# Optimization experiments

Hardware: AMD Instinct MI355X
Metric: run time of the kernel (lower is better)

The kernel has to match this reference:

```python
import jax, jax.numpy as jnp
import numpy as np


def gcn_conv(x, W, b, src, dst, dinv_sqrt, n_nodes):
    # PyG GCNConv: h = X W; out_i = sum_j norm_ij * h_j + b, norm = d_i^-1/2 d_j^-1/2
    h = x @ W  # [N, out]
    norm = dinv_sqrt[src] * dinv_sqrt[dst]  # [E]
    msg = h[src] * norm[:, None]  # [E, out]
    out = jax.ops.segment_sum(msg, dst, num_segments=n_nodes)
    return out + b


def setup_inputs() -> dict:
    key = jax.random.key(0)
    ks = jax.random.split(key, 12)
    N, E, G = 50000, 400000, 512
    x = jax.random.normal(ks[0], (N, 3), dtype=jnp.float32)
    edge_index = jax.random.randint(ks[1], (2, E), 0, N, dtype=jnp.int64)
    batch = jnp.sort(jax.random.randint(ks[2], (N,), 0, G, dtype=jnp.int64))
    def lin(k, fin, fout):
        kw, kb = jax.random.split(k)
        s = 1.0 / np.sqrt(fin)
        return (jax.random.uniform(kw, (fin, fout), jnp.float32, -s, s),
                jax.random.uniform(kb, (fout,), jnp.float32, -s, s))
    W1, b1 = lin(ks[3], 3, 100)
    W2, b2 = lin(ks[4], 100, 200)
    W3, b3 = lin(ks[5], 200, 100)
    W4, b4 = lin(ks[6], 100, 1)
    return {"x": x, "edge_index": edge_index, "batch": batch, "num_graphs": G,
            "W1": W1, "b1": b1, "W2": W2, "b2": b2,
            "W3": W3, "b3": b3, "W4": W4, "b4": b4}


def reference(x, edge_index, batch, num_graphs, W1, b1, W2, b2, W3, b3, W4, b4):
    N = x.shape[0]
    loop = jnp.arange(N, dtype=edge_index.dtype)
    src = jnp.concatenate([edge_index[0], loop])  # self-loops added (GCNConv default)
    dst = jnp.concatenate([edge_index[1], loop])
    deg = jax.ops.segment_sum(jnp.ones_like(src, dtype=x.dtype), dst, num_segments=N)
    dinv_sqrt = deg ** -0.5  # deg >= 1 due to self-loops

    h = jax.nn.silu(gcn_conv(x, W1, b1, src, dst, dinv_sqrt, N))
    h = jax.nn.silu(gcn_conv(h, W2, b2, src, dst, dinv_sqrt, N))

    # global_mean_pool over `batch` segments
    sums = jax.ops.segment_sum(h, batch, num_segments=num_graphs)  # [G, 200]
    cnts = jax.ops.segment_sum(jnp.ones((N,), h.dtype), batch, num_segments=num_graphs)
    pooled = sums / jnp.maximum(cnts, 1.0)[:, None]

    h = jax.nn.silu(pooled @ W3 + b3)
    out = h @ W4 + b4  # [G, 1]
    return out.squeeze(-1)
```

## Files before the change

kernel.cpp:

```cpp
#include <hip/hip_runtime.h>
#include <math.h>

#define WF 64

__device__ __forceinline__ float silu_f(float v){ return v / (1.0f + expf(-v)); }

typedef __attribute__((ext_vector_type(8))) short bf16x8;
typedef __attribute__((ext_vector_type(4))) float f32x4;

__device__ __forceinline__ void bf16split(float v, unsigned short& h, unsigned short& l){
  unsigned int b = __float_as_uint(v);
  unsigned int hh = (b + 0x8000u) >> 16;
  float hf = __uint_as_float(hh << 16);
  float lo = v - hf;
  unsigned int bl = __float_as_uint(lo);
  h = (unsigned short)hh;
  l = (unsigned short)((bl + 0x8000u) >> 16);
}

__global__ __launch_bounds__(256) void k_count(const int* __restrict__ dst, int* __restrict__ cnt, int E){
  int e = blockIdx.x*blockDim.x + threadIdx.x;
  if (e < E) atomicAdd(&cnt[dst[e]], 1);
}

__global__ __launch_bounds__(256) void k_scan1(const int* __restrict__ cnt, int* __restrict__ rowstart, int* __restrict__ bsum, int N){
  __shared__ int s[256];
  int tid = threadIdx.x;
  int base = blockIdx.x*2048 + tid*8;
  int loc[8]; int tsum = 0;
#pragma unroll
  for (int j=0;j<8;++j){ int idx=base+j; int v = (idx<N)?cnt[idx]:0; loc[j]=tsum; tsum+=v; }
  s[tid]=tsum; __syncthreads();
  for (int off=1; off<256; off<<=1){
    int v = (tid>=off)? s[tid-off] : 0;
    __syncthreads();
    s[tid] += v;
    __syncthreads();
  }
  int texc = s[tid] - tsum;
  if (tid==255) bsum[blockIdx.x] = s[255];
#pragma unroll
  for (int j=0;j<8;++j){ int idx=base+j; if (idx<N) rowstart[idx] = texc + loc[j]; }
}

__global__ __launch_bounds__(256) void k_scan3(const int* __restrict__ bsum, const int* __restrict__ cnt,
                        const float* __restrict__ x,
                        int* __restrict__ rowstart, int* __restrict__ cursor,
                        float* __restrict__ dinv, float4* __restrict__ dxp,
                        int N, int E, int nb){
  __shared__ int boffs;
  int tid = threadIdx.x;
  int b = (blockIdx.x*blockDim.x) >> 11;
  if (tid < WF){
    int v = (tid < nb && tid < b) ? bsum[tid] : 0;
#pragma unroll
    for (int off=32; off; off>>=1) v += __shfl_down(v, off);
    if (tid==0) boffs = v;
  }
  __syncthreads();
  int idx = blockIdx.x*blockDim.x + tid;
  if (idx < N){
    int v = rowstart[idx] + boffs;
    rowstart[idx]=v; cursor[idx]=v;
    float di = rsqrtf((float)(cnt[idx]+1));
    dinv[idx] = di;
    float4 o;
    o.x = di;
    o.y = di*x[3*idx+0];
    o.z = di*x[3*idx+1];
    o.w = di*x[3*idx+2];
    dxp[idx] = o;
  }
  if (idx==0) rowstart[N]=E;
}

__global__ __launch_bounds__(256) void k_fill(const int* __restrict__ src, const int* __restrict__ dst,
                       int* __restrict__ cursor, int* __restrict__ colsrc, int E){
  int e = blockIdx.x*blockDim.x + threadIdx.x;
  if (e < E){
    int d = dst[e];
    int pos = atomicAdd(&cursor[d], 1);
    colsrc[pos] = src[e];
  }
}

__global__ __launch_bounds__(256) void k_wconv(const float* __restrict__ W2,
                       unsigned short* __restrict__ w2th, unsigned short* __restrict__ w2tl){
  int idx = blockIdx.x*blockDim.x + threadIdx.x;
  if (idx < 224*128){
    int f = idx >> 7, k = idx & 127;
    float v = (f < 200 && k < 100) ? W2[(size_t)k*200 + f] : 0.f;
    unsigned short h, l;
    bf16split(v, h, l);
    w2th[idx] = h;
    w2tl[idx] = l;
  }
}

__global__ __launch_bounds__(256) void k_l1(const float4* __restrict__ dxp,
                     const int* __restrict__ rowstart, const int* __restrict__ colsrc,
                     const float* __restrict__ W1, const float* __restrict__ b1,
                     float* __restrict__ h1s, int N){
  __shared__ float w[300];
  __shared__ float bb[100];
  int tid = threadIdx.x;
  for (int t=tid; t<300; t+=blockDim.x) w[t]=W1[t];
  for (int t=tid; t<100; t+=blockDim.x) bb[t]=b1[t];
  __syncthreads();
  int i = blockIdx.x*blockDim.x + tid;
  if (i >= N) return;
  float4 self = dxp[i];
  float di = self.x;
  float sx = self.y, sy = self.z, sz = self.w;
  int jb = rowstart[i], je = rowstart[i+1];
  int j = jb;
  for (; j+3 < je; j += 4){
    float4 r0 = dxp[colsrc[j]];
    float4 r1 = dxp[colsrc[j+1]];
    float4 r2 = dxp[colsrc[j+2]];
    float4 r3 = dxp[colsrc[j+3]];
    sx += (r0.y + r1.y) + (r2.y + r3.y);
    sy += (r0.z + r1.z) + (r2.z + r3.z);
    sz += (r0.w + r1.w) + (r2.w + r3.w);
  }
  for (; j < je; ++j){
    float4 r = dxp[colsrc[j]];
    sx += r.y; sy += r.z; sz += r.w;
  }
  sx*=di; sy*=di; sz*=di;
  float* orow = h1s + (size_t)i*100;
#pragma unroll
  for (int f0=0; f0<100; f0+=4){
    float4 o;
    o.x = silu_f(sx*w[f0+0] + sy*w[100+f0+0] + sz*w[200+f0+0] + bb[f0+0]);
    o.y = silu_f(sx*w[f0+1] + sy*w[100+f0+1] + sz*w[200+f0+1] + bb[f0+1]);
    o.z = silu_f(sx*w[f0+2] + sy*w[100+f0+2] + sz*w[200+f0+2] + bb[f0+2]);
    o.w = silu_f(sx*w[f0+3] + sy*w[100+f0+3] + sz*w[200+f0+3] + bb[f0+3]);
    *(float4*)&orow[f0] = o;
  }
}

__global__ __launch_bounds__(256) void k_agg2(const float* __restrict__ h1s, const int* __restrict__ rowstart,
                       const int* __restrict__ colsrc, const float* __restrict__ dinv,
                       unsigned short* __restrict__ a2h, unsigned short* __restrict__ a2l, int N){
  int node = blockIdx.x*8 + (threadIdx.x >> 5);
  int lane = threadIdx.x & 31;
  if (node >= N) return;
  if (lane >= 25){
    int ko = 100 + (lane-25)*4;
    ushort4 z = make_ushort4(0,0,0,0);
    *(ushort4*)(a2h + (size_t)node*128 + ko) = z;
    *(ushort4*)(a2l + (size_t)node*128 + ko) = z;
    return;
  }
  float di = dinv[node];
  float4 v = *(const float4*)(h1s + (size_t)node*100 + lane*4);
  float4 acc;
  acc.x = di*v.x; acc.y = di*v.y; acc.z = di*v.z; acc.w = di*v.w;
  int jb = rowstart[node], je = rowstart[node+1];
  int j = jb;
  for (; j+1 < je; j += 2){
    int u0 = colsrc[j];   float w0 = dinv[u0];
    int u1 = colsrc[j+1]; float w1 = dinv[u1];
    float4 r0 = *(const float4*)(h1s + (size_t)u0*100 + lane*4);
    float4 r1 = *(const float4*)(h1s + (size_t)u1*100 + lane*4);
    acc.x += w0*r0.x + w1*r1.x;
    acc.y += w0*r0.y + w1*r1.y;
    acc.z += w0*r0.z + w1*r1.z;
    acc.w += w0*r0.w + w1*r1.w;
  }
  if (j < je){
    int u = colsrc[j]; float wv = dinv[u];
    float4 r = *(const float4*)(h1s + (size_t)u*100 + lane*4);
    acc.x += wv*r.x; acc.y += wv*r.y; acc.z += wv*r.z; acc.w += wv*r.w;
  }
  float o[4] = { di*acc.x, di*acc.y, di*acc.z, di*acc.w };
  ushort4 h4, l4;
  bf16split(o[0], h4.x, l4.x);
  bf16split(o[1], h4.y, l4.y);
  bf16split(o[2], h4.z, l4.z);
  bf16split(o[3], h4.w, l4.w);
  *(ushort4*)(a2h + (size_t)node*128 + lane*4) = h4;
  *(ushort4*)(a2l + (size_t)node*128 + lane*4) = l4;
}

__global__ __launch_bounds__(256) void k_mm2(const unsigned short* __restrict__ a2h,
                      const unsigned short* __restrict__ a2l,
                      const unsigned short* __restrict__ w2th,
                      const unsigned short* __restrict__ w2tl,
                      const float* __restrict__ b2, const int* __restrict__ batch,
                      float* __restrict__ pooled, int N){
  __shared__ float plL[256];
  int tid = threadIdx.x;
  int l = tid & 63, w = tid >> 6;
  int n0 = blockIdx.x * 64;
  int fb = blockIdx.y;
  int row = l & 15;
  int kg  = l >> 4;

  const unsigned short* ah_p = a2h + (size_t)(n0 + w*16 + row)*128;
  const unsigned short* al_p = a2l + (size_t)(n0 + w*16 + row)*128;
  int gf0 = fb*32 + row, gf1 = gf0 + 16;
  const unsigned short* wh0_p = w2th + (size_t)gf0*128;
  const unsigned short* wl0_p = w2tl + (size_t)gf0*128;
  const unsigned short* wh1_p = w2th + (size_t)gf1*128;
  const unsigned short* wl1_p = w2tl + (size_t)gf1*128;

  f32x4 acc0 = {0.f,0.f,0.f,0.f};
  f32x4 acc1 = {0.f,0.f,0.f,0.f};
#pragma unroll
  for (int ks = 0; ks < 4; ++ks){
    int ko = ks*32 + kg*8;
    bf16x8 ah  = *(const bf16x8*)(ah_p  + ko);
    bf16x8 al  = *(const bf16x8*)(al_p  + ko);
    bf16x8 wh0 = *(const bf16x8*)(wh0_p + ko);
    bf16x8 wl0 = *(const bf16x8*)(wl0_p + ko);
    bf16x8 wh1 = *(const bf16x8*)(wh1_p + ko);
    bf16x8 wl1 = *(const bf16x8*)(wl1_p + ko);
    acc0 = __builtin_amdgcn_mfma_f32_16x16x32_bf16(ah, wh0, acc0, 0, 0, 0);
    acc0 = __builtin_amdgcn_mfma_f32_16x16x32_bf16(ah, wl0, acc0, 0, 0, 0);
    acc0 = __builtin_amdgcn_mfma_f32_16x16x32_bf16(al, wh0, acc0, 0, 0, 0);
    acc1 = __builtin_amdgcn_mfma_f32_16x16x32_bf16(ah, wh1, acc1, 0, 0, 0);
    acc1 = __builtin_amdgcn_mfma_f32_16x16x32_bf16(ah, wl1, acc1, 0, 0, 0);
    acc1 = __builtin_amdgcn_mfma_f32_16x16x32_bf16(al, wh1, acc1, 0, 0, 0);
  }

  plL[tid] = 0.f;
  __syncthreads();

  int g0 = batch[n0];
#pragma unroll
  for (int ft = 0; ft < 2; ++ft){
    f32x4 a = ft ? acc1 : acc0;
    int fl = ft*16 + row;
    int gf = fb*32 + fl;
    if (gf < 200){
      float bias = b2[gf];
      float s = 0.f;
      int gprev = -1;
#pragma unroll
      for (int r = 0; r < 4; ++r){
        int node = n0 + w*16 + kg*4 + r;
        if (node < N){
          int g = batch[node];
          if (g != gprev){
            if (gprev >= 0){
              int dg = gprev - g0;
              if (dg < 8) atomicAdd(&plL[dg*32 + fl], s);
              else        atomicAdd(&pooled[(size_t)gprev*200 + gf], s);
            }
            gprev = g; s = 0.f;
          }
          s += silu_f(a[r] + bias);
        }
      }
      if (gprev >= 0){
        int dg = gprev - g0;
        if (dg < 8) atomicAdd(&plL[dg*32 + fl], s);
        else        atomicAdd(&pooled[(size_t)gprev*200 + gf], s);
      }
    }
  }
  __syncthreads();
  {
    float v = plL[tid];
    if (v != 0.f){
      int r = tid >> 5, f = tid & 31;
      int gf = fb*32 + f;
      if (gf < 200) atomicAdd(&pooled[(size_t)(g0+r)*200 + gf], v);
    }
  }
}

__global__ __launch_bounds__(256) void k_head(const float* __restrict__ pooled, const int* __restrict__ batch,
                       const float* __restrict__ W3, const float* __restrict__ b3,
                       const float* __restrict__ W4, const float* __restrict__ b4,
                       float* __restrict__ out, int N){
  __shared__ float pl[200];
  __shared__ float h3[100];
  int g = blockIdx.x; int tid = threadIdx.x;
  int lo=0, hi=N;
  while (lo<hi){ int m=(lo+hi)>>1; if (batch[m] < g) lo=m+1; else hi=m; }
  int s = lo;
  hi=N;
  while (lo<hi){ int m=(lo+hi)>>1; if (batch[m] < g+1) lo=m+1; else hi=m; }
  int e = lo;
  float inv = (e>s) ? 1.0f/(float)(e-s) : 0.0f;
  if (tid < 200) pl[tid] = pooled[(size_t)g*200 + tid] * inv;
  __syncthreads();
  if (tid < 100){
    float acc = b3[tid];
    for (int k=0;k<200;++k) acc += pl[k]*W3[k*100+tid];
    h3[tid] = silu_f(acc);
  }
  __syncthreads();
  if (tid < WF){
    float p = 0.f;
    if (tid < 100)      p  = h3[tid]     * W4[tid];
    if (tid + 64 < 100) p += h3[tid+64]  * W4[tid+64];
#pragma unroll
    for (int off=32; off; off>>=1) p += __shfl_down(p, off);
    if (tid==0) out[g] = p + b4[0];
  }
}

extern "C" void kernel_launch(void* const* d_in, const int* in_sizes, int n_in,
                              void* d_out, int out_size, void* d_ws, size_t ws_size,
                              hipStream_t stream){
  const float* x  = (const float*)d_in[0];
  const int*   ei = (const int*)  d_in[1];
  const int* batch= (const int*)  d_in[2];
  const float* W1 = (const float*)d_in[4];
  const float* b1 = (const float*)d_in[5];
  const float* W2 = (const float*)d_in[6];
  const float* b2 = (const float*)d_in[7];
  const float* W3 = (const float*)d_in[8];
  const float* b3 = (const float*)d_in[9];
  const float* W4 = (const float*)d_in[10];
  const float* b4 = (const float*)d_in[11];
  float* out = (float*)d_out;

  int N = in_sizes[0]/3;
  int E = in_sizes[1]/2;
  int G = out_size;
  const int* src = ei;
  const int* dst = ei + E;
  int NP = ((N + 63)/64)*64;

  char* base = (char*)d_ws; size_t off = 0;
  auto alloc = [&](size_t bytes)->void*{
    void* p = base + off;
    off = (off + bytes + 255) & ~(size_t)255;
    return p;
  };
  int*   cnt      = (int*)  alloc((size_t)N*4);
  float* pooled   = (float*)alloc((size_t)G*200*4);
  size_t zbytes   = off;
  int*   rowstart = (int*)  alloc((size_t)(N+1)*4);
  int*   cursor   = (int*)  alloc((size_t)N*4);
  int*   bsum     = (int*)  alloc(4096);
  int*   colsrc   = (int*)  alloc((size_t)E*4);
  float* dinv     = (float*)alloc((size_t)N*4);
  float4* dxp     = (float4*)alloc((size_t)N*16);
  float* h1s      = (float*)alloc((size_t)N*100*4);
  unsigned short* a2h = (unsigned short*)alloc((size_t)NP*128*2);
  unsigned short* a2l = (unsigned short*)alloc((size_t)NP*128*2);
  unsigned short* w2th = (unsigned short*)alloc((size_t)224*128*2);
  unsigned short* w2tl = (unsigned short*)alloc((size_t)224*128*2);
  (void)ws_size; (void)n_in;

  hipMemsetAsync(base, 0, zbytes, stream);
  int gE = (E+255)/256;
  k_count<<<gE,256,0,stream>>>(dst, cnt, E);
  int nb = (N+2047)/2048;
  k_scan1<<<nb,256,0,stream>>>(cnt, rowstart, bsum, N);
  k_scan3<<<(N+255)/256,256,0,stream>>>(bsum, cnt, x, rowstart, cursor, dinv, dxp, N, E, nb);
  k_wconv<<<(224*128+255)/256,256,0,stream>>>(W2, w2th, w2tl);
  k_fill<<<gE,256,0,stream>>>(src, dst, cursor, colsrc, E);
  k_l1<<<(N+255)/256,256,0,stream>>>(dxp, rowstart, colsrc, W1, b1, h1s, N);
  k_agg2<<<(N+7)/8,256,0,stream>>>(h1s, rowstart, colsrc, dinv, a2h, a2l, N);
  dim3 gmm((N+63)/64, 7);
  k_mm2<<<gmm,256,0,stream>>>(a2h, a2l, w2th, w2tl, b2, batch, pooled, N);
  k_head<<<G,256,0,stream>>>(pooled, batch, W3, b3, W4, b4, out, N);
}
```

Measured before the change: 182.4 us.

## Loop over all feature blocks in k_mm2 to reuse A fragments in registers

k_mm2 used to launch a 2D grid where each block handled 64 nodes by one 32-feature slice, so every feature slice reloaded the a2h/a2l activation rows from global memory. Each 128-thread block now handles 32 nodes, loads their A fragments into registers once, and loops over all 7 feature blocks. Weight fragments are reloaded per iteration from the small, cache-resident W2 arrays. The cost is a serial loop with extra barriers per feature block and fewer total blocks, which reduces parallelism and latency hiding.

```diff
diff --git a/kernel.cpp b/kernel.cpp
--- a/kernel.cpp
+++ b/kernel.cpp
@@ -184,7 +184,7 @@
   *(ushort4*)(a2l + (size_t)node*128 + lane*4) = l4;
 }
 
-__global__ __launch_bounds__(256) void k_mm2(const unsigned short* __restrict__ a2h,
+__global__ __launch_bounds__(128) void k_mm2(const unsigned short* __restrict__ a2h,
                       const unsigned short* __restrict__ a2l,
                       const unsigned short* __restrict__ w2th,
                       const unsigned short* __restrict__ w2tl,
@@ -193,81 +193,91 @@
   __shared__ float plL[256];
   int tid = threadIdx.x;
   int l = tid & 63, w = tid >> 6;
-  int n0 = blockIdx.x * 64;
-  int fb = blockIdx.y;
+  int n0 = blockIdx.x * 32;
   int row = l & 15;
   int kg  = l >> 4;
 
   const unsigned short* ah_p = a2h + (size_t)(n0 + w*16 + row)*128;
   const unsigned short* al_p = a2l + (size_t)(n0 + w*16 + row)*128;
-  int gf0 = fb*32 + row, gf1 = gf0 + 16;
-  const unsigned short* wh0_p = w2th + (size_t)gf0*128;
-  const unsigned short* wl0_p = w2tl + (size_t)gf0*128;
-  const unsigned short* wh1_p = w2th + (size_t)gf1*128;
-  const unsigned short* wl1_p = w2tl + (size_t)gf1*128;
-
-  f32x4 acc0 = {0.f,0.f,0.f,0.f};
-  f32x4 acc1 = {0.f,0.f,0.f,0.f};
+
+  bf16x8 ahf[4], alf[4];
 #pragma unroll
   for (int ks = 0; ks < 4; ++ks){
     int ko = ks*32 + kg*8;
-    bf16x8 ah  = *(const bf16x8*)(ah_p  + ko);
-    bf16x8 al  = *(const bf16x8*)(al_p  + ko);
-    bf16x8 wh0 = *(const bf16x8*)(wh0_p + ko);
-    bf16x8 wl0 = *(const bf16x8*)(wl0_p + ko);
-    bf16x8 wh1 = *(const bf16x8*)(wh1_p + ko);
-    bf16x8 wl1 = *(const bf16x8*)(wl1_p + ko);
-    acc0 = __builtin_amdgcn_mfma_f32_16x16x32_bf16(ah, wh0, acc0, 0, 0, 0);
-    acc0 = __builtin_amdgcn_mfma_f32_16x16x32_bf16(ah, wl0, acc0, 0, 0, 0);
-    acc0 = __builtin_amdgcn_mfma_f32_16x16x32_bf16(al, wh0, acc0, 0, 0, 0);
-    acc1 = __builtin_amdgcn_mfma_f32_16x16x32_bf16(ah, wh1, acc1, 0, 0, 0);
-    acc1 = __builtin_amdgcn_mfma_f32_16x16x32_bf16(ah, wl1, acc1, 0, 0, 0);
-    acc1 = __builtin_amdgcn_mfma_f32_16x16x32_bf16(al, wh1, acc1, 0, 0, 0);
-  }
-
-  plL[tid] = 0.f;
-  __syncthreads();
+    ahf[ks] = *(const bf16x8*)(ah_p + ko);
+    alf[ks] = *(const bf16x8*)(al_p + ko);
+  }
 
   int g0 = batch[n0];
-#pragma unroll
-  for (int ft = 0; ft < 2; ++ft){
-    f32x4 a = ft ? acc1 : acc0;
-    int fl = ft*16 + row;
-    int gf = fb*32 + fl;
-    if (gf < 200){
-      float bias = b2[gf];
-      float s = 0.f;
-      int gprev = -1;
-#pragma unroll
-      for (int r = 0; r < 4; ++r){
-        int node = n0 + w*16 + kg*4 + r;
-        if (node < N){
-          int g = batch[node];
-          if (g != gprev){
-            if (gprev >= 0){
-              int dg = gprev - g0;
-              if (dg < 8) atomicAdd(&plL[dg*32 + fl], s);
-              else        atomicAdd(&pooled[(size_t)gprev*200 + gf], s);
+
+  for (int fb = 0; fb < 7; ++fb){
+    int gf0 = fb*32 + row, gf1 = gf0 + 16;
+    const unsigned short* wh0_p = w2th + (size_t)gf0*128;
+    const unsigned short* wl0_p = w2tl + (size_t)gf0*128;
+    const unsigned short* wh1_p = w2th + (size_t)gf1*128;
+    const unsigned short* wl1_p = w2tl + (size_t)gf1*128;
+
+    f32x4 acc0 = {0.f,0.f,0.f,0.f};
+    f32x4 acc1 = {0.f,0.f,0.f,0.f};
+#pragma unroll
+    for (int ks = 0; ks < 4; ++ks){
+      int ko = ks*32 + kg*8;
+      bf16x8 wh0 = *(const bf16x8*)(wh0_p + ko);
+      bf16x8 wl0 = *(const bf16x8*)(wl0_p + ko);
+      bf16x8 wh1 = *(const bf16x8*)(wh1_p + ko);
+      bf16x8 wl1 = *(const bf16x8*)(wl1_p + ko);
+      acc0 = __builtin_amdgcn_mfma_f32_16x16x32_bf16(ahf[ks], wh0, acc0, 0, 0, 0);
+      acc0 = __builtin_amdgcn_mfma_f32_16x16x32_bf16(ahf[ks], wl0, acc0, 0, 0, 0);
+      acc0 = __builtin_amdgcn_mfma_f32_16x16x32_bf16(alf[ks], wh0, acc0, 0, 0, 0);
+      acc1 = __builtin_amdgcn_mfma_f32_16x16x32_bf16(ahf[ks], wh1, acc1, 0, 0, 0);
+      acc1 = __builtin_amdgcn_mfma_f32_16x16x32_bf16(ahf[ks], wl1, acc1, 0, 0, 0);
+      acc1 = __builtin_amdgcn_mfma_f32_16x16x32_bf16(alf[ks], wh1, acc1, 0, 0, 0);
+    }
+
+    __syncthreads();
+    for (int idx = tid; idx < 256; idx += 128) plL[idx] = 0.f;
+    __syncthreads();
+
+#pragma unroll
+    for (int ft = 0; ft < 2; ++ft){
+      f32x4 a = ft ? acc1 : acc0;
+      int fl = ft*16 + row;
+      int gf = fb*32 + fl;
+      if (gf < 200){
+        float bias = b2[gf];
+        float s = 0.f;
+        int gprev = -1;
+#pragma unroll
+        for (int r = 0; r < 4; ++r){
+          int node = n0 + w*16 + kg*4 + r;
+          if (node < N){
+            int g = batch[node];
+            if (g != gprev){
+              if (gprev >= 0){
+                int dg = gprev - g0;
+                if (dg < 8) atomicAdd(&plL[dg*32 + fl], s);
+                else        atomicAdd(&pooled[(size_t)gprev*200 + gf], s);
+              }
+              gprev = g; s = 0.f;
             }
-            gprev = g; s = 0.f;
+            s += silu_f(a[r] + bias);
           }
-          s += silu_f(a[r] + bias);
+        }
+        if (gprev >= 0){
+          int dg = gprev - g0;
+          if (dg < 8) atomicAdd(&plL[dg*32 + fl], s);
+          else        atomicAdd(&pooled[(size_t)gprev*200 + gf], s);
         }
       }
-      if (gprev >= 0){
-        int dg = gprev - g0;
-        if (dg < 8) atomicAdd(&plL[dg*32 + fl], s);
-        else        atomicAdd(&pooled[(size_t)gprev*200 + gf], s);
+    }
+    __syncthreads();
+    for (int idx = tid; idx < 256; idx += 128){
+      float v = plL[idx];
+      if (v != 0.f){
+        int r = idx >> 5, f = idx & 31;
+        int gf = fb*32 + f;
+        if (gf < 200) atomicAdd(&pooled[(size_t)(g0+r)*200 + gf], v);
       }
-    }
-  }
-  __syncthreads();
-  {
-    float v = plL[tid];
-    if (v != 0.f){
-      int r = tid >> 5, f = tid & 31;
-      int gf = fb*32 + f;
-      if (gf < 200) atomicAdd(&pooled[(size_t)(g0+r)*200 + gf], v);
     }
   }
 }
@@ -359,7 +369,6 @@
   k_fill<<<gE,256,0,stream>>>(src, dst, cursor, colsrc, E);
   k_l1<<<(N+255)/256,256,0,stream>>>(dxp, rowstart, colsrc, W1, b1, h1s, N);
   k_agg2<<<(N+7)/8,256,0,stream>>>(h1s, rowstart, colsrc, dinv, a2h, a2l, N);
-  dim3 gmm((N+63)/64, 7);
-  k_mm2<<<gmm,256,0,stream>>>(a2h, a2l, w2th, w2tl, b2, batch, pooled, N);
+  k_mm2<<<(N+31)/32,128,0,stream>>>(a2h, a2l, w2th, w2tl, b2, batch, pooled, N);
   k_head<<<G,256,0,stream>>>(pooled, batch, W3, b3, W4, b4, out, N);
 }
```

Result: slower. 189.3 us (+3.7%).
